# Kernel optimization log

Measured on AMD Instinct MI355X. Metric: run time of the kernel, lower is better.

The kernel has to match this reference:

```python
import jax, jax.numpy as jnp
import numpy as np

NUM_HEADS = 8
NUM_GROUPS = 8
EPS = 1e-5


def setup_inputs() -> dict:
    key = jax.random.key(0)
    k1, k2, k3 = jax.random.split(key, 3)
    B, C, H, W = 16, 512, 32, 32
    x = jax.random.normal(k1, (B, C, H, W), dtype=jnp.float32)
    gn_w = jnp.ones((C,), jnp.float32)
    gn_b = jnp.zeros((C,), jnp.float32)
    # 1x1 convs are plain GEMMs; scale weights like torch default init (~1/sqrt(C))
    qkv_w = jax.random.normal(k2, (3 * C, C), dtype=jnp.float32) * (1.0 / np.sqrt(C))
    qkv_b = jnp.zeros((3 * C,), jnp.float32)
    proj_w = jax.random.normal(k3, (C, C), dtype=jnp.float32) * (1.0 / np.sqrt(C))
    proj_b = jnp.zeros((C,), jnp.float32)
    return {"x": x, "gn_w": gn_w, "gn_b": gn_b, "qkv_w": qkv_w,
            "qkv_b": qkv_b, "proj_w": proj_w, "proj_b": proj_b}


def _group_norm(x, w, b):
    B, C, H, W = x.shape
    xg = x.reshape(B, NUM_GROUPS, -1)  # [B, G, (C/G)*H*W]
    mu = xg.mean(axis=-1, keepdims=True)
    var = xg.var(axis=-1, keepdims=True)
    xn = ((xg - mu) * jax.lax.rsqrt(var + EPS)).reshape(B, C, H, W)
    return xn * w[None, :, None, None] + b[None, :, None, None]


def reference(x, gn_w, gn_b, qkv_w, qkv_b, proj_w, proj_b):
    B, C, H, W = x.shape
    nh = NUM_HEADS
    d = C // nh
    xn = _group_norm(x, gn_w, gn_b)
    # 1x1 conv == channel GEMM
    qkv = jnp.einsum('oc,bchw->bohw', qkv_w, xn) + qkv_b[None, :, None, None]
    qkv = qkv.reshape(B, 3, nh, d, H * W)
    q, k, v = qkv[:, 0], qkv[:, 1], qkv[:, 2]  # [B, nh, d, N]
    scale = d ** (-0.5)
    attn = jax.nn.softmax(jnp.einsum('bhdi,bhdj->bhij', q, k) * scale, axis=-1)
    o = jnp.einsum('bhij,bhdj->bhdi', attn, v).reshape(B, C, H, W)
    # NOTE: source reassigns x, so residual uses attention output, not input
    return o + (jnp.einsum('oc,bchw->bohw', proj_w, o) + proj_b[None, :, None, None])
```

## Files before the change

kernel.cpp:

```cpp
#include <hip/hip_runtime.h>
#include <math.h>

typedef unsigned short u16;
typedef __attribute__((ext_vector_type(8))) short bf8;
typedef __attribute__((ext_vector_type(4))) short s4v;
typedef __attribute__((ext_vector_type(4))) float f4;

#define MFMA(a, b, c) __builtin_amdgcn_mfma_f32_16x16x32_bf16(a, b, c, 0, 0, 0)

#if defined(__has_builtin)
#if __has_builtin(__builtin_amdgcn_exp2f)
#define EXP2(x) __builtin_amdgcn_exp2f(x)
#endif
#endif
#ifndef EXP2
#define EXP2(x) exp2f(x)
#endif

__device__ __forceinline__ u16 f2bf(float f) {
    unsigned u = __float_as_uint(f);
    u += 0x7fffu + ((u >> 16) & 1u);
    return (u16)(u >> 16);
}
__device__ __forceinline__ float bf2f(u16 h) {
    return __uint_as_float(((unsigned)h) << 16);
}
__device__ __forceinline__ void split2(float v, u16& h, u16& l) {
    h = f2bf(v);
    l = f2bf(v - bf2f(h));
}
__device__ __forceinline__ void ldg_lds16(const u16* g, u16* l) {
    __builtin_amdgcn_global_load_lds(
        (const __attribute__((address_space(1))) unsigned int*)g,
        (__attribute__((address_space(3))) unsigned int*)l, 16, 0, 0);
}

__global__ __launch_bounds__(256) void gn_partial(
    const float* __restrict__ x, float2* __restrict__ partial)
{
    const int p = blockIdx.x;
    const float4* x4 = (const float4*)x + (size_t)p * 2048;
    const int tid = threadIdx.x;
    float s = 0.f, ss = 0.f;
    for (int i = tid; i < 2048; i += 256) {
        float4 v = x4[i];
        s  += v.x + v.y + v.z + v.w;
        ss += v.x*v.x + v.y*v.y + v.z*v.z + v.w*v.w;
    }
    for (int off = 32; off > 0; off >>= 1) {
        s  += __shfl_down(s, off);
        ss += __shfl_down(ss, off);
    }
    __shared__ float red[8];
    const int wvi = tid >> 6;
    if ((tid & 63) == 0) { red[wvi] = s; red[4 + wvi] = ss; }
    __syncthreads();
    if (tid == 0)
        partial[p] = make_float2(red[0] + red[1] + red[2] + red[3],
                                 red[4] + red[5] + red[6] + red[7]);
}

__global__ void gn_reduce(const float2* __restrict__ partial,
                          float2* __restrict__ stats)
{
    const int g = threadIdx.x;
    if (g < 128) {
        float s = 0.f, ss = 0.f;
        #pragma unroll
        for (int i = 0; i < 8; ++i) {
            float2 p = partial[g*8 + i];
            s += p.x; ss += p.y;
        }
        const float inv = 1.f / 65536.f;
        const float mu = s * inv;
        const float var = ss * inv - mu * mu;
        stats[g] = make_float2(mu, rsqrtf(var + 1e-5f));
    }
}

__global__ __launch_bounds__(256) void gn_apply(
    const float* __restrict__ x, const float* __restrict__ gw,
    const float* __restrict__ gb, const float2* __restrict__ stats,
    u16* __restrict__ xh)
{
    const int blk = blockIdx.x;
    const int bg = blk >> 3, sc = (blk & 7) * 128;
    const int b = bg >> 3, g = bg & 7;
    const size_t base = (size_t)bg * 65536;
    const float2 st = stats[bg];
    const float mu = st.x, rstd = st.y;
    const int tid = threadIdx.x;

    __shared__ float tile[64][65];
    for (int s0 = sc; s0 < sc + 128; s0 += 64) {
        for (int idx = tid; idx < 1024; idx += 256) {
            const int c = idx >> 4, s4i = (idx & 15) * 4;
            const float w = gw[g*64 + c], bb = gb[g*64 + c];
            float4 v = *(const float4*)&x[base + (size_t)c*1024 + s0 + s4i];
            tile[s4i + 0][c] = (v.x - mu)*rstd*w + bb;
            tile[s4i + 1][c] = (v.y - mu)*rstd*w + bb;
            tile[s4i + 2][c] = (v.z - mu)*rstd*w + bb;
            tile[s4i + 3][c] = (v.w - mu)*rstd*w + bb;
        }
        __syncthreads();
        for (int idx = tid; idx < 1024; idx += 256) {
            const int srow = idx >> 4, c4 = (idx & 15) * 4;
            s4v hv;
            #pragma unroll
            for (int j = 0; j < 4; ++j)
                hv[j] = (short)f2bf(tile[srow][c4 + j]);
            const size_t o = ((size_t)b*1024 + s0 + srow)*512 + g*64 + c4;
            *(s4v*)&xh[o] = hv;
        }
        __syncthreads();
    }
}

__global__ __launch_bounds__(256) void prep_w(
    const float* __restrict__ wq, const float* __restrict__ wp,
    u16* __restrict__ qwh, u16* __restrict__ pwh)
{
    const int i = blockIdx.x * 256 + threadIdx.x;
    if (i < 786432) {
        qwh[i] = f2bf(wq[i]);
    } else {
        const int j = i - 786432;
        pwh[j] = f2bf(wp[j]);
    }
}

__global__ __launch_bounds__(256, 4) void qkv_mfma(
    const u16* __restrict__ Ah, const u16* __restrict__ Bh,
    const float* __restrict__ bias,
    u16* __restrict__ qh, u16* __restrict__ kh, u16* __restrict__ vh)
{
    __shared__ u16 smem[2*8192];
    const int tid = threadIdx.x;
    const int wv = tid >> 6, ln = tid & 63;
    const int lr = ln & 15, lg = ln >> 4;
    const int m0 = blockIdx.x * 128;
    const int n0 = blockIdx.y * 128;
    const int b  = blockIdx.z;
    const size_t Abase = ((size_t)b*1024 + m0) * 512;
    const size_t Bbase = (size_t)n0 * 512;
    const int wm = (wv >> 1) * 64, wn = (wv & 1) * 64;
    const int srr = ln >> 3, sg = ln & 7;

    f4 acc[4][4] = {};

    for (int k0 = 0; k0 < 512; k0 += 64) {
        __syncthreads();
        #pragma unroll
        for (int it = 0; it < 8; ++it) {
            const int chunk = wv*8 + it;
            const int plane = chunk >> 4;
            const int row = ((chunk & 15) << 3) + srr;
            const u16* srcp = (plane == 0) ? (Ah + Abase) : (Bh + Bbase);
            const u16* gp = srcp + (size_t)row*512 + k0 + ((sg ^ (row & 7)) << 3);
            ldg_lds16(gp, smem + chunk*512);
        }
        __syncthreads();
        #pragma unroll
        for (int f = 0; f < 2; ++f) {
            bf8 av[4], b0[4];
            #pragma unroll
            for (int mf = 0; mf < 4; ++mf) {
                const int row = wm + mf*16 + lr;
                const int ch = (f*4 + lg) ^ (row & 7);
                av[mf] = *(const bf8*)&smem[row*64 + (ch << 3)];
            }
            #pragma unroll
            for (int nf = 0; nf < 4; ++nf) {
                const int row = wn + nf*16 + lr;
                const int ch = (f*4 + lg) ^ (row & 7);
                b0[nf] = *(const bf8*)&smem[8192 + row*64 + (ch << 3)];
            }
            #pragma unroll
            for (int mf = 0; mf < 4; ++mf)
                #pragma unroll
                for (int nf = 0; nf < 4; ++nf)
                    acc[mf][nf] = MFMA(av[mf], b0[nf], acc[mf][nf]);
        }
    }

    #pragma unroll
    for (int nf = 0; nf < 4; ++nf) {
        const int o = n0 + wn + nf*16 + lr;
        const int which = o >> 9;
        const int hd = (o >> 6) & 7;
        const int dd = o & 63;
        const float bs = bias[o];
        const int bh = b*8 + hd;
        #pragma unroll
        for (int mf = 0; mf < 4; ++mf) {
            const int s = m0 + wm + mf*16 + lg*4;
            if (which == 2) {
                s4v hv;
                #pragma unroll
                for (int r = 0; r < 4; ++r)
                    hv[r] = (short)f2bf(acc[mf][nf][r] + bs);
                const size_t a = ((size_t)bh*64 + dd)*1024 + s;
                *(s4v*)&vh[a] = hv;
            } else {
                const float sc = (which == 0) ? 0.18033688011112042f : 1.f;
                u16* dst = (which == 0) ? qh : kh;
                const size_t a = ((size_t)bh*1024 + s)*64 + dd;
                #pragma unroll
                for (int r = 0; r < 4; ++r)
                    dst[a + (size_t)r*64] = f2bf((acc[mf][nf][r] + bs)*sc);
            }
        }
    }
}

__global__ __launch_bounds__(256, 3) void attn_mfma(
    const u16* __restrict__ qh_, const u16* __restrict__ kh_,
    const u16* __restrict__ vh_,
    u16* __restrict__ oh_, u16* __restrict__ ol_)
{
    __shared__ u16 Kt[2][64][64];
    __shared__ u16 Vt[2][64][64];
    __shared__ u16 Pt[4][2][16][72];
    const int tid = threadIdx.x;
    const int wv = tid >> 6, ln = tid & 63;
    const int lr = ln & 15, lg = ln >> 4;
    const int flat = blockIdx.x + (blockIdx.y << 3);
    const int bh = ((flat & 7) << 4) + (flat >> 6);
    const int q0 = ((flat >> 3) & 7) * 128;
    const size_t qkb = (size_t)bh * 65536;
    const int srr = ln >> 3, sg = ln & 7;

    bf8 qf[2][2];
    #pragma unroll
    for (int ii = 0; ii < 2; ++ii)
        #pragma unroll
        for (int f = 0; f < 2; ++f)
            qf[ii][f] = *(const bf8*)&qh_[qkb
                + (size_t)(q0 + wv*32 + ii*16 + lr)*64 + f*32 + lg*8];

    float lpart[2] = {0.f, 0.f};
    f4 oacc[2][4] = {};

    #pragma unroll
    for (int it = 0; it < 4; ++it) {
        const int chunk = wv*4 + it;
        const int row = (chunk & 7)*8 + srr;
        const u16* gp = (chunk < 8)
            ? kh_ + qkb + (size_t)row*64 + ((sg ^ (row & 7)) << 3)
            : vh_ + qkb + (size_t)row*1024 + ((sg ^ (row & 7)) << 3);
        u16* dst = ((chunk < 8) ? &Kt[0][0][0] : &Vt[0][0][0]) + (chunk & 7)*512;
        ldg_lds16(gp, dst);
    }

    for (int t = 0; t < 16; ++t) {
        const int cur = t & 1;
        const int j0 = t * 64;
        const u16* kbuf = &Kt[cur][0][0];
        const u16* vbuf = &Vt[cur][0][0];

        asm volatile("s_waitcnt vmcnt(0)" ::: "memory");
        __syncthreads();

        if (t < 15) {
            #pragma unroll
            for (int it = 0; it < 4; ++it) {
                const int chunk = wv*4 + it;
                const int row = (chunk & 7)*8 + srr;
                const u16* gp = (chunk < 8)
                    ? kh_ + qkb + (size_t)(j0 + 64 + row)*64
                          + ((sg ^ (row & 7)) << 3)
                    : vh_ + qkb + (size_t)row*1024 + j0 + 64
                          + ((sg ^ (row & 7)) << 3);
                u16* dst = ((chunk < 8) ? &Kt[cur^1][0][0] : &Vt[cur^1][0][0])
                           + (chunk & 7)*512;
                ldg_lds16(gp, dst);
            }
        }

        #pragma unroll
        for (int ii = 0; ii < 2; ++ii) {
            f4 sacc[4] = {};
            #pragma unroll
            for (int jf = 0; jf < 4; ++jf)
                #pragma unroll
                for (int f = 0; f < 2; ++f) {
                    const int row = jf*16 + lr;
                    const int ch = (f*4 + lg) ^ (row & 7);
                    const bf8 kv = *(const bf8*)&kbuf[row*64 + (ch << 3)];
                    sacc[jf] = MFMA(kv, qf[ii][f], sacc[jf]);
                }

            float ps = 0.f;
            #pragma unroll
            for (int jf = 0; jf < 4; ++jf) {
                s4v hv;
                #pragma unroll
                for (int r = 0; r < 4; ++r) {
                    const float p = EXP2(sacc[jf][r]);
                    ps += p;
                    hv[r] = (short)(__float_as_uint(p) >> 16);
                }
                *(s4v*)&Pt[wv][ii][lr][(jf*4 + lg)*4] = hv;
            }
            lpart[ii] += ps;

            #pragma unroll
            for (int f = 0; f < 2; ++f) {
                const bf8 pa = *(const bf8*)&Pt[wv][ii][lr][(f*4 + lg)*8];
                #pragma unroll
                for (int nf = 0; nf < 4; ++nf) {
                    const int row = nf*16 + lr;
                    const int ch = (f*4 + lg) ^ (row & 7);
                    const bf8 vv = *(const bf8*)&vbuf[row*64 + (ch << 3)];
                    oacc[ii][nf] = MFMA(pa, vv, oacc[ii][nf]);
                }
            }
        }
    }

    #pragma unroll
    for (int ii = 0; ii < 2; ++ii) {
        lpart[ii] += __shfl_xor(lpart[ii], 16);
        lpart[ii] += __shfl_xor(lpart[ii], 32);
    }

    const int b = bh >> 3, h = bh & 7;
    #pragma unroll
    for (int ii = 0; ii < 2; ++ii) {
        float inv[4];
        #pragma unroll
        for (int r = 0; r < 4; ++r)
            inv[r] = 1.f / __shfl(lpart[ii], lg*4 + r);
        #pragma unroll
        for (int nf = 0; nf < 4; ++nf) {
            const int dd = nf*16 + lr;
            #pragma unroll
            for (int r = 0; r < 4; ++r) {
                const int s = q0 + wv*32 + ii*16 + lg*4 + r;
                const float val = oacc[ii][nf][r] * inv[r];
                const size_t a = ((size_t)b*1024 + s)*512 + h*64 + dd;
                u16 hh, ll; split2(val, hh, ll);
                oh_[a] = hh;
                ol_[a] = ll;
            }
        }
    }
}

__global__ __launch_bounds__(256, 4) void proj_mfma(
    const u16* __restrict__ Ah, const u16* __restrict__ Al,
    const u16* __restrict__ Bh,
    const float* __restrict__ bias, float* __restrict__ out)
{
    __shared__ u16 smem[2*8192];
    const int tid = threadIdx.x;
    const int wv = tid >> 6, ln = tid & 63;
    const int lr = ln & 15, lg = ln >> 4;
    const int m0 = blockIdx.x * 128;
    const int n0 = blockIdx.y * 128;
    const int b  = blockIdx.z;
    const size_t Abase = ((size_t)b*1024 + m0) * 512;
    const size_t Bbase = (size_t)n0 * 512;
    const int wm = (wv >> 1) * 64, wn = (wv & 1) * 64;
    const int srr = ln >> 3, sg = ln & 7;

    f4 acc[4][4] = {};

    for (int k0 = 0; k0 < 512; k0 += 64) {
        __syncthreads();
        #pragma unroll
        for (int it = 0; it < 8; ++it) {
            const int chunk = wv*8 + it;
            const int plane = chunk >> 4;
            const int row = ((chunk & 15) << 3) + srr;
            const u16* srcp = (plane == 0) ? (Ah + Abase) : (Bh + Bbase);
            const u16* gp = srcp + (size_t)row*512 + k0 + ((sg ^ (row & 7)) << 3);
            ldg_lds16(gp, smem + chunk*512);
        }
        __syncthreads();
        #pragma unroll
        for (int f = 0; f < 2; ++f) {
            bf8 av[4], b0[4];
            #pragma unroll
            for (int mf = 0; mf < 4; ++mf) {
                const int row = wm + mf*16 + lr;
                const int ch = (f*4 + lg) ^ (row & 7);
                av[mf] = *(const bf8*)&smem[row*64 + (ch << 3)];
            }
            #pragma unroll
            for (int nf = 0; nf < 4; ++nf) {
                const int row = wn + nf*16 + lr;
                const int ch = (f*4 + lg) ^ (row & 7);
                b0[nf] = *(const bf8*)&smem[8192 + row*64 + (ch << 3)];
            }
            #pragma unroll
            for (int mf = 0; mf < 4; ++mf)
                #pragma unroll
                for (int nf = 0; nf < 4; ++nf)
                    acc[mf][nf] = MFMA(av[mf], b0[nf], acc[mf][nf]);
        }
    }

    #pragma unroll
    for (int nf = 0; nf < 4; ++nf) {
        const int o = n0 + wn + nf*16 + lr;
        const float bs = bias[o];
        #pragma unroll
        for (int mf = 0; mf < 4; ++mf) {
            const int s = m0 + wm + mf*16 + lg*4;
            const size_t ob = ((size_t)b*1024 + s)*512 + o;
            float4 r;
            r.x = acc[mf][nf][0] + bs + bf2f(Ah[ob])         + bf2f(Al[ob]);
            r.y = acc[mf][nf][1] + bs + bf2f(Ah[ob + 512])   + bf2f(Al[ob + 512]);
            r.z = acc[mf][nf][2] + bs + bf2f(Ah[ob + 1024])  + bf2f(Al[ob + 1024]);
            r.w = acc[mf][nf][3] + bs + bf2f(Ah[ob + 1536])  + bf2f(Al[ob + 1536]);
            *(float4*)&out[((size_t)b*512 + o)*1024 + s] = r;
        }
    }
}

extern "C" void kernel_launch(void* const* d_in, const int* in_sizes, int n_in,
                              void* d_out, int out_size, void* d_ws, size_t ws_size,
                              hipStream_t stream) {
    const float* x      = (const float*)d_in[0];
    const float* gn_w   = (const float*)d_in[1];
    const float* gn_b   = (const float*)d_in[2];
    const float* qkv_w  = (const float*)d_in[3];
    const float* qkv_b  = (const float*)d_in[4];
    const float* proj_w = (const float*)d_in[5];
    const float* proj_b = (const float*)d_in[6];
    float* out = (float*)d_out;

    u16* w = (u16*)d_ws;
    const size_t P = 8388608UL;
    u16* xh = w;
    u16* ol = w + P;
    u16* qh = w + 2*P;
    u16* pwh = w + 3*P;
    u16* kh = w + 4*P;
    u16* vh = w + 6*P;
    u16* oh = xh;
    u16* qwh = (u16*)d_out;
    float2* partial = (float2*)(w + 5*P);
    float2* stats   = partial + 1024;

    hipLaunchKernelGGL(prep_w, dim3(4096), dim3(256), 0, stream,
                       qkv_w, proj_w, qwh, pwh);
    hipLaunchKernelGGL(gn_partial, dim3(1024), dim3(256), 0, stream, x, partial);
    hipLaunchKernelGGL(gn_reduce, dim3(1), dim3(128), 0, stream, partial, stats);
    hipLaunchKernelGGL(gn_apply, dim3(1024), dim3(256), 0, stream,
                       x, gn_w, gn_b, stats, xh);
    hipLaunchKernelGGL(qkv_mfma, dim3(8, 12, 16), dim3(256), 0, stream,
                       xh, qwh, qkv_b, qh, kh, vh);
    hipLaunchKernelGGL(attn_mfma, dim3(8, 128), dim3(256), 0, stream,
                       qh, kh, vh, oh, ol);
    hipLaunchKernelGGL(proj_mfma, dim3(8, 4, 16), dim3(256), 0, stream,
                       oh, ol, pwh, proj_b, out);
}
```

Measured before the change: 133.8 us.

## Use 32x32 MFMA in attention with register P exchange; fuse prep kernels

The attention kernel moves from 16x16x32 to 32x32x16 bf16 MFMA. The softmax probabilities are repacked into the A operand with cross-half lane shuffles instead of a round trip through shared memory, so the Pt buffer is removed and the occupancy hint rises to 4. The row sums are shared through a small LDS array for final normalization. Separately, weight conversion is merged into the GN partial-sum launch and the single-block gn_reduce is folded into gn_apply, cutting two kernel launches at the cost of some redundant stat recomputation.

After: 131.2 us. About the same (-2.0%).

```diff
diff --git a/kernel.cpp b/kernel.cpp
--- a/kernel.cpp
+++ b/kernel.cpp
@@ -5,8 +5,10 @@
 typedef __attribute__((ext_vector_type(8))) short bf8;
 typedef __attribute__((ext_vector_type(4))) short s4v;
 typedef __attribute__((ext_vector_type(4))) float f4;
-
-#define MFMA(a, b, c) __builtin_amdgcn_mfma_f32_16x16x32_bf16(a, b, c, 0, 0, 0)
+typedef __attribute__((ext_vector_type(16))) float f16v;
+
+#define MFMA(a, b, c)   __builtin_amdgcn_mfma_f32_16x16x32_bf16(a, b, c, 0, 0, 0)
+#define MFMA32(a, b, c) __builtin_amdgcn_mfma_f32_32x32x16_bf16(a, b, c, 0, 0, 0)
 
 #if defined(__has_builtin)
 #if __has_builtin(__builtin_amdgcn_exp2f)
@@ -29,18 +31,29 @@
     h = f2bf(v);
     l = f2bf(v - bf2f(h));
 }
+__device__ __forceinline__ unsigned pk2(float a, float b) {
+    return (__float_as_uint(a) >> 16) | (__float_as_uint(b) & 0xffff0000u);
+}
 __device__ __forceinline__ void ldg_lds16(const u16* g, u16* l) {
     __builtin_amdgcn_global_load_lds(
         (const __attribute__((address_space(1))) unsigned int*)g,
         (__attribute__((address_space(3))) unsigned int*)l, 16, 0, 0);
 }
 
-__global__ __launch_bounds__(256) void gn_partial(
-    const float* __restrict__ x, float2* __restrict__ partial)
+__global__ __launch_bounds__(256) void gn_partial_prep(
+    const float* __restrict__ x, float2* __restrict__ partial,
+    const float* __restrict__ wq, const float* __restrict__ wp,
+    u16* __restrict__ qwh, u16* __restrict__ pwh)
 {
+    const int tid = threadIdx.x;
+    if (blockIdx.x >= 1024) {
+        const int i = (blockIdx.x - 1024) * 256 + tid;
+        if (i < 786432) qwh[i] = f2bf(wq[i]);
+        else            pwh[i - 786432] = f2bf(wp[i - 786432]);
+        return;
+    }
     const int p = blockIdx.x;
     const float4* x4 = (const float4*)x + (size_t)p * 2048;
-    const int tid = threadIdx.x;
     float s = 0.f, ss = 0.f;
     for (int i = tid; i < 2048; i += 256) {
         float4 v = x4[i];
@@ -60,35 +73,23 @@
                                  red[4] + red[5] + red[6] + red[7]);
 }
 
-__global__ void gn_reduce(const float2* __restrict__ partial,
-                          float2* __restrict__ stats)
-{
-    const int g = threadIdx.x;
-    if (g < 128) {
-        float s = 0.f, ss = 0.f;
-        #pragma unroll
-        for (int i = 0; i < 8; ++i) {
-            float2 p = partial[g*8 + i];
-            s += p.x; ss += p.y;
-        }
-        const float inv = 1.f / 65536.f;
-        const float mu = s * inv;
-        const float var = ss * inv - mu * mu;
-        stats[g] = make_float2(mu, rsqrtf(var + 1e-5f));
-    }
-}
-
 __global__ __launch_bounds__(256) void gn_apply(
     const float* __restrict__ x, const float* __restrict__ gw,
-    const float* __restrict__ gb, const float2* __restrict__ stats,
+    const float* __restrict__ gb, const float2* __restrict__ partial,
     u16* __restrict__ xh)
 {
     const int blk = blockIdx.x;
     const int bg = blk >> 3, sc = (blk & 7) * 128;
     const int b = bg >> 3, g = bg & 7;
     const size_t base = (size_t)bg * 65536;
-    const float2 st = stats[bg];
-    const float mu = st.x, rstd = st.y;
+    float s = 0.f, ss = 0.f;
+    #pragma unroll
+    for (int i = 0; i < 8; ++i) {
+        float2 pp = partial[bg*8 + i];
+        s += pp.x; ss += pp.y;
+    }
+    const float mu = s * (1.f / 65536.f);
+    const float rstd = rsqrtf(ss * (1.f / 65536.f) - mu * mu + 1e-5f);
     const int tid = threadIdx.x;
 
     __shared__ float tile[64][65];
@@ -113,19 +114,6 @@
             *(s4v*)&xh[o] = hv;
         }
         __syncthreads();
-    }
-}
-
-__global__ __launch_bounds__(256) void prep_w(
-    const float* __restrict__ wq, const float* __restrict__ wp,
-    u16* __restrict__ qwh, u16* __restrict__ pwh)
-{
-    const int i = blockIdx.x * 256 + threadIdx.x;
-    if (i < 786432) {
-        qwh[i] = f2bf(wq[i]);
-    } else {
-        const int j = i - 786432;
-        pwh[j] = f2bf(wp[j]);
     }
 }
 
@@ -213,33 +201,31 @@
     }
 }
 
-__global__ __launch_bounds__(256, 3) void attn_mfma(
+__global__ __launch_bounds__(256, 4) void attn_mfma(
     const u16* __restrict__ qh_, const u16* __restrict__ kh_,
     const u16* __restrict__ vh_,
     u16* __restrict__ oh_, u16* __restrict__ ol_)
 {
     __shared__ u16 Kt[2][64][64];
     __shared__ u16 Vt[2][64][64];
-    __shared__ u16 Pt[4][2][16][72];
+    __shared__ float lsh[4][32];
     const int tid = threadIdx.x;
     const int wv = tid >> 6, ln = tid & 63;
-    const int lr = ln & 15, lg = ln >> 4;
+    const int l31 = ln & 31, L = ln >> 5;
     const int flat = blockIdx.x + (blockIdx.y << 3);
     const int bh = ((flat & 7) << 4) + (flat >> 6);
     const int q0 = ((flat >> 3) & 7) * 128;
     const size_t qkb = (size_t)bh * 65536;
     const int srr = ln >> 3, sg = ln & 7;
 
-    bf8 qf[2][2];
-    #pragma unroll
-    for (int ii = 0; ii < 2; ++ii)
-        #pragma unroll
-        for (int f = 0; f < 2; ++f)
-            qf[ii][f] = *(const bf8*)&qh_[qkb
-                + (size_t)(q0 + wv*32 + ii*16 + lr)*64 + f*32 + lg*8];
-
-    float lpart[2] = {0.f, 0.f};
-    f4 oacc[2][4] = {};
+    bf8 qf[4];
+    #pragma unroll
+    for (int dk = 0; dk < 4; ++dk)
+        qf[dk] = *(const bf8*)&qh_[qkb
+            + (size_t)(q0 + wv*32 + l31)*64 + dk*16 + L*8];
+
+    float lpart = 0.f;
+    f16v oacc[2] = {};
 
     #pragma unroll
     for (int it = 0; it < 4; ++it) {
@@ -278,71 +264,67 @@
         }
 
         #pragma unroll
-        for (int ii = 0; ii < 2; ++ii) {
-            f4 sacc[4] = {};
-            #pragma unroll
-            for (int jf = 0; jf < 4; ++jf)
+        for (int jb = 0; jb < 2; ++jb) {
+            f16v sacc = {};
+            #pragma unroll
+            for (int dk = 0; dk < 4; ++dk) {
+                const int row = jb*32 + l31;
+                const int ch = (dk*2 + L) ^ (row & 7);
+                const bf8 kv = *(const bf8*)&kbuf[row*64 + (ch << 3)];
+                sacc = MFMA32(kv, qf[dk], sacc);
+            }
+            float p[16];
+            float ps = 0.f;
+            #pragma unroll
+            for (int r = 0; r < 16; ++r) { p[r] = EXP2(sacc[r]); ps += p[r]; }
+            lpart += ps;
+
+            #pragma unroll
+            for (int h = 0; h < 2; ++h) {
+                const int bse = h*8;
+                const unsigned lo0 = pk2(p[bse+0], p[bse+1]);
+                const unsigned lo1 = pk2(p[bse+2], p[bse+3]);
+                const unsigned hi0 = pk2(p[bse+4], p[bse+5]);
+                const unsigned hi1 = pk2(p[bse+6], p[bse+7]);
+                const unsigned e0 = L ? lo0 : hi0;
+                const unsigned e1 = L ? lo1 : hi1;
+                const unsigned r0 = __shfl_xor(e0, 32);
+                const unsigned r1 = __shfl_xor(e1, 32);
+                unsigned pu[4];
+                pu[0] = L ? r0 : lo0;
+                pu[1] = L ? r1 : lo1;
+                pu[2] = L ? hi0 : r0;
+                pu[3] = L ? hi1 : r1;
+                const bf8 pa = *(const bf8*)pu;
                 #pragma unroll
-                for (int f = 0; f < 2; ++f) {
-                    const int row = jf*16 + lr;
-                    const int ch = (f*4 + lg) ^ (row & 7);
-                    const bf8 kv = *(const bf8*)&kbuf[row*64 + (ch << 3)];
-                    sacc[jf] = MFMA(kv, qf[ii][f], sacc[jf]);
+                for (int dn = 0; dn < 2; ++dn) {
+                    const int d = dn*32 + l31;
+                    const int jcb = (jb*2 + h)*2 + L;
+                    const int ch = jcb ^ (d & 7);
+                    const bf8 vvf = *(const bf8*)&vbuf[d*64 + (ch << 3)];
+                    oacc[dn] = MFMA32(pa, vvf, oacc[dn]);
                 }
-
-            float ps = 0.f;
-            #pragma unroll
-            for (int jf = 0; jf < 4; ++jf) {
-                s4v hv;
-                #pragma unroll
-                for (int r = 0; r < 4; ++r) {
-                    const float p = EXP2(sacc[jf][r]);
-                    ps += p;
-                    hv[r] = (short)(__float_as_uint(p) >> 16);
-                }
-                *(s4v*)&Pt[wv][ii][lr][(jf*4 + lg)*4] = hv;
-            }
-            lpart[ii] += ps;
-
-            #pragma unroll
-            for (int f = 0; f < 2; ++f) {
-                const bf8 pa = *(const bf8*)&Pt[wv][ii][lr][(f*4 + lg)*8];
-                #pragma unroll
-                for (int nf = 0; nf < 4; ++nf) {
-                    const int row = nf*16 + lr;
-                    const int ch = (f*4 + lg) ^ (row & 7);
-                    const bf8 vv = *(const bf8*)&vbuf[row*64 + (ch << 3)];
-                    oacc[ii][nf] = MFMA(pa, vv, oacc[ii][nf]);
-                }
-            }
-        }
-    }
-
-    #pragma unroll
-    for (int ii = 0; ii < 2; ++ii) {
-        lpart[ii] += __shfl_xor(lpart[ii], 16);
-        lpart[ii] += __shfl_xor(lpart[ii], 32);
-    }
+            }
+        }
+    }
+
+    lpart += __shfl_xor(lpart, 32);
+    if (L == 0) lsh[wv][l31] = lpart;
 
     const int b = bh >> 3, h = bh & 7;
     #pragma unroll
-    for (int ii = 0; ii < 2; ++ii) {
-        float inv[4];
-        #pragma unroll
-        for (int r = 0; r < 4; ++r)
-            inv[r] = 1.f / __shfl(lpart[ii], lg*4 + r);
-        #pragma unroll
-        for (int nf = 0; nf < 4; ++nf) {
-            const int dd = nf*16 + lr;
-            #pragma unroll
-            for (int r = 0; r < 4; ++r) {
-                const int s = q0 + wv*32 + ii*16 + lg*4 + r;
-                const float val = oacc[ii][nf][r] * inv[r];
-                const size_t a = ((size_t)b*1024 + s)*512 + h*64 + dd;
-                u16 hh, ll; split2(val, hh, ll);
-                oh_[a] = hh;
-                ol_[a] = ll;
-            }
+    for (int dn = 0; dn < 2; ++dn) {
+        #pragma unroll
+        for (int r = 0; r < 16; ++r) {
+            const int irow = (r & 3) + 8*(r >> 2) + 4*L;
+            const float inv = 1.f / lsh[wv][irow];
+            const float val = oacc[dn][r] * inv;
+            const int s = q0 + wv*32 + irow;
+            const int dd = dn*32 + l31;
+            const size_t a = ((size_t)b*1024 + s)*512 + h*64 + dd;
+            u16 hh, ll; split2(val, hh, ll);
+            oh_[a] = hh;
+            ol_[a] = ll;
         }
     }
 }
@@ -442,14 +424,11 @@
     u16* oh = xh;
     u16* qwh = (u16*)d_out;
     float2* partial = (float2*)(w + 5*P);
-    float2* stats   = partial + 1024;
-
-    hipLaunchKernelGGL(prep_w, dim3(4096), dim3(256), 0, stream,
-                       qkv_w, proj_w, qwh, pwh);
-    hipLaunchKernelGGL(gn_partial, dim3(1024), dim3(256), 0, stream, x, partial);
-    hipLaunchKernelGGL(gn_reduce, dim3(1), dim3(128), 0, stream, partial, stats);
+
+    hipLaunchKernelGGL(gn_partial_prep, dim3(5120), dim3(256), 0, stream,
+                       x, partial, qkv_w, proj_w, qwh, pwh);
     hipLaunchKernelGGL(gn_apply, dim3(1024), dim3(256), 0, stream,
-                       x, gn_w, gn_b, stats, xh);
+                       x, gn_w, gn_b, partial, xh);
     hipLaunchKernelGGL(qkv_mfma, dim3(8, 12, 16), dim3(256), 0, stream,
                        xh, qwh, qkv_b, qh, kh, vh);
     hipLaunchKernelGGL(attn_mfma, dim3(8, 128), dim3(256), 0, stream,
```
